# Performance work log

Hardware: AMD Instinct MI355X
Metric: run time of the kernel (lower is better)

## Reference

```python
import jax, jax.numpy as jnp
import numpy as np

D_MODEL = 512
NUM_HEADS = 8
NUM_REL_EMB = 1024


def _linear(x, w, b):
    # torch nn.Linear convention: w is [out, in]
    return x @ w.T + b


def setup_inputs() -> dict:
    key = jax.random.key(0)
    B, S, D = 1, 512, D_MODEL
    ks = jax.random.split(key, 14)
    scale = D ** -0.5
    def w(i):
        return jax.random.normal(ks[i], (D, D), jnp.float32) * scale
    def b(i):
        return jax.random.normal(ks[i], (D,), jnp.float32) * 0.01
    return {
        "hidden_states": jax.random.normal(ks[0], (B, S, D), jnp.float32),
        "emb_table": jax.random.normal(ks[1], (NUM_REL_EMB, D), jnp.float32) * 0.02,
        "wq": w(2), "bq": b(3),
        "wk": w(4), "bk": b(5),
        "wv": w(6), "bv": b(7),
        "wrk": w(8), "brk": b(9),
        "wrq": w(10), "brq": b(11),
        "wo": w(12), "bo": b(13),
    }


def reference(hidden_states, emb_table, wq, bq, wk, bk, wv, bv,
              wrk, brk, wrq, brq, wo, bo):
    B, S, D = hidden_states.shape
    H = NUM_HEADS
    hd = D // H
    NE = emb_table.shape[0]

    # relative positions j - i, shifted and clamped, then embedded: [S, S, D]
    rel_pos = jnp.arange(S)[None, :] - jnp.arange(S)[:, None]
    idx = jnp.clip(rel_pos + NE // 2, 0, NE - 1)
    rel_emb = emb_table[idx]  # [S, S, D] (identical across batch)

    q = _linear(hidden_states, wq, bq).reshape(B, S, H, hd).transpose(0, 2, 1, 3)  # [B,H,S,hd]
    k = _linear(hidden_states, wk, bk).reshape(B, S, H, hd).transpose(0, 2, 1, 3)
    v = _linear(hidden_states, wv, bv).reshape(B, S, H, hd).transpose(0, 2, 1, 3)

    rk = _linear(rel_emb, wrk, brk).reshape(S, S, H, hd)  # [i, j, H, hd]
    rq = _linear(rel_emb, wrq, brq).reshape(S, S, H, hd)

    # content-content + content-relative + relative-content scores: [B,H,S,S]
    scores = (
        jnp.einsum('bhid,bhjd->bhij', q, k)
        + jnp.einsum('bhid,ijhd->bhij', q, rk)
        + jnp.einsum('ijhd,bhjd->bhij', rq, k)
    )

    attn = jax.nn.softmax(scores / jnp.sqrt(jnp.asarray(hd, scores.dtype)), axis=-1)
    # dropout is identity (p=0.0 / eval mode)

    ctx = jnp.einsum('bhij,bhjd->bhid', attn, v)          # [B,H,S,hd]
    ctx = ctx.transpose(0, 2, 1, 3).reshape(B, S, D)       # merge heads
    out = _linear(ctx, wo, bo)
    return out, attn
```

## Files before the change

kernel.cpp:

```cpp
#include <hip/hip_runtime.h>
#include <stdint.h>


typedef __bf16 bf16_t;
typedef bf16_t bf16x8 __attribute__((ext_vector_type(8)));
typedef float f32x4 __attribute__((ext_vector_type(4)));

__device__ __forceinline__ uint16_t f2bf(float f) {
  union { float f; uint32_t i; } c; c.f = f;
  return (uint16_t)((c.i + 0x7fffu + ((c.i >> 16) & 1u)) >> 16);
}
__device__ __forceinline__ uint32_t pack2bf(float lo, float hi) {
  return (uint32_t)f2bf(lo) | ((uint32_t)f2bf(hi) << 16);
}
#define MFMA(a, b, c) __builtin_amdgcn_mfma_f32_16x16x32_bf16((a), (b), (c), 0, 0, 0)

#define LSTR 40
#define SSTR 72

__global__ __launch_bounds__(256) void gemm_bt_kernel(
    const void* __restrict__ A, int lda, int zsA, int aF32,
    const void* __restrict__ B, int ldb, int zsB, int bF32,
    const float* __restrict__ bias, int hasBias,
    float* __restrict__ C, int ldc, int zsC, int K)
{
  __shared__ __align__(16) uint16_t As[64 * LSTR];
  __shared__ __align__(16) uint16_t Bs[64 * LSTR];
  const int z = blockIdx.z;
  const int m0 = blockIdx.y * 64, n0 = blockIdx.x * 64;
  const int t = threadIdx.x, lane = t & 63, wave = t >> 6;
  const int wi = wave & 1, wj = wave >> 1;
  const int quad = lane >> 4, l15 = lane & 15;
  const int srow = t >> 2, scol = (t & 3) * 8;

  f32x4 acc[2][2] = {};
  for (int k0 = 0; k0 < K; k0 += 32) {
    uint4 ap, bp;
    if (aF32) {
      const float* Af = (const float*)A + (size_t)z * zsA + (size_t)(m0 + srow) * lda + (k0 + scol);
      float4 x0 = *(const float4*)(Af); float4 x1 = *(const float4*)(Af + 4);
      ap.x = pack2bf(x0.x, x0.y); ap.y = pack2bf(x0.z, x0.w);
      ap.z = pack2bf(x1.x, x1.y); ap.w = pack2bf(x1.z, x1.w);
    } else {
      ap = *(const uint4*)((const uint16_t*)A + (size_t)z * zsA + (size_t)(m0 + srow) * lda + (k0 + scol));
    }
    if (bF32) {
      const float* Bf = (const float*)B + (size_t)z * zsB + (size_t)(n0 + srow) * ldb + (k0 + scol);
      float4 x0 = *(const float4*)(Bf); float4 x1 = *(const float4*)(Bf + 4);
      bp.x = pack2bf(x0.x, x0.y); bp.y = pack2bf(x0.z, x0.w);
      bp.z = pack2bf(x1.x, x1.y); bp.w = pack2bf(x1.z, x1.w);
    } else {
      bp = *(const uint4*)((const uint16_t*)B + (size_t)z * zsB + (size_t)(n0 + srow) * ldb + (k0 + scol));
    }
    *(uint4*)(&As[srow * LSTR + scol]) = ap;
    *(uint4*)(&Bs[srow * LSTR + scol]) = bp;
    __syncthreads();
    bf16x8 af[2], bfr[2];
#pragma unroll
    for (int x = 0; x < 2; x++) {
      af[x]  = *(const bf16x8*)(&As[(wi * 32 + x * 16 + l15) * LSTR + quad * 8]);
      bfr[x] = *(const bf16x8*)(&Bs[(wj * 32 + x * 16 + l15) * LSTR + quad * 8]);
    }
#pragma unroll
    for (int x = 0; x < 2; x++)
#pragma unroll
      for (int y = 0; y < 2; y++)
        acc[x][y] = MFMA(af[x], bfr[y], acc[x][y]);
    __syncthreads();
  }
#pragma unroll
  for (int x = 0; x < 2; x++)
#pragma unroll
    for (int y = 0; y < 2; y++) {
      const int j = n0 + wj * 32 + y * 16 + l15;
      const float bval = hasBias ? bias[j] : 0.0f;
      const int ib = m0 + wi * 32 + x * 16 + quad * 4;
#pragma unroll
      for (int r = 0; r < 4; r++)
        C[(size_t)z * zsC + (size_t)(ib + r) * ldc + j] = acc[x][y][r] + bval;
    }
}

__global__ __launch_bounds__(256) void proj_kernel(
    const float* __restrict__ X, const float* __restrict__ emb,
    const float* __restrict__ wq, const float* __restrict__ bq,
    const float* __restrict__ wk, const float* __restrict__ bk,
    const float* __restrict__ wv, const float* __restrict__ bv,
    const float* __restrict__ wrk, const float* __restrict__ brk,
    const float* __restrict__ wrq, const float* __restrict__ brq,
    uint16_t* __restrict__ q, uint16_t* __restrict__ k, uint16_t* __restrict__ vT,
    uint16_t* __restrict__ rkE, uint16_t* __restrict__ rqE)
{
  int bid = blockIdx.x;
  const float *A, *B, *bias; uint16_t* C; int mode;
  if (bid < 64)       {            A = X;   B = wq;  bias = bq;  C = q;   mode = 2; }
  else if (bid < 128) { bid -= 64; A = X;   B = wk;  bias = bk;  C = k;   mode = 2; }
  else if (bid < 192) { bid -= 128; A = X;  B = wv;  bias = bv;  C = vT;  mode = 3; }
  else if (bid < 320) { bid -= 192; A = emb; B = wrk; bias = brk; C = rkE; mode = 1; }
  else                { bid -= 320; A = emb; B = wrq; bias = brq; C = rqE; mode = 1; }
  const int m0 = (bid >> 3) * 64, n0 = (bid & 7) * 64;

  __shared__ __align__(16) uint16_t As[64 * LSTR];
  __shared__ __align__(16) uint16_t Bs[64 * LSTR];
  const int t = threadIdx.x, lane = t & 63, wave = t >> 6;
  const int wi = wave & 1, wj = wave >> 1;
  const int quad = lane >> 4, l15 = lane & 15;
  const int srow = t >> 2, scol = (t & 3) * 8;

  f32x4 acc[2][2] = {};
  for (int k0 = 0; k0 < 512; k0 += 32) {
    const float* Af = A + (size_t)(m0 + srow) * 512 + (k0 + scol);
    const float* Bf = B + (size_t)(n0 + srow) * 512 + (k0 + scol);
    float4 a0 = *(const float4*)(Af), a1 = *(const float4*)(Af + 4);
    float4 b0 = *(const float4*)(Bf), b1 = *(const float4*)(Bf + 4);
    uint4 ap, bp;
    ap.x = pack2bf(a0.x, a0.y); ap.y = pack2bf(a0.z, a0.w);
    ap.z = pack2bf(a1.x, a1.y); ap.w = pack2bf(a1.z, a1.w);
    bp.x = pack2bf(b0.x, b0.y); bp.y = pack2bf(b0.z, b0.w);
    bp.z = pack2bf(b1.x, b1.y); bp.w = pack2bf(b1.z, b1.w);
    *(uint4*)(&As[srow * LSTR + scol]) = ap;
    *(uint4*)(&Bs[srow * LSTR + scol]) = bp;
    __syncthreads();
    bf16x8 af[2], bfr[2];
#pragma unroll
    for (int x = 0; x < 2; x++) {
      af[x]  = *(const bf16x8*)(&As[(wi * 32 + x * 16 + l15) * LSTR + quad * 8]);
      bfr[x] = *(const bf16x8*)(&Bs[(wj * 32 + x * 16 + l15) * LSTR + quad * 8]);
    }
#pragma unroll
    for (int x = 0; x < 2; x++)
#pragma unroll
      for (int y = 0; y < 2; y++)
        acc[x][y] = MFMA(af[x], bfr[y], acc[x][y]);
    __syncthreads();
  }
#pragma unroll
  for (int x = 0; x < 2; x++)
#pragma unroll
    for (int y = 0; y < 2; y++) {
      const int j = n0 + wj * 32 + y * 16 + l15;
      const float bval = bias[j];
      const int ib = m0 + wi * 32 + x * 16 + quad * 4;
#pragma unroll
      for (int r = 0; r < 4; r++) {
        const int i = ib + r;
        size_t off;
        if (mode == 1)      off = (size_t)i * 512 + j;
        else if (mode == 2) off = (size_t)(j >> 6) * 32768 + (size_t)i * 64 + (size_t)(j & 63);
        else                off = (size_t)(j >> 6) * 32768 + (size_t)(j & 63) * 512 + (size_t)i;
        C[off] = f2bf(acc[x][y][r] + bval);
      }
    }
}

__global__ __launch_bounds__(256) void scores_kernel(
    const uint16_t* __restrict__ q, const uint16_t* __restrict__ k,
    const uint16_t* __restrict__ rkE, const uint16_t* __restrict__ rqE,
    float* __restrict__ S)
{
  __shared__ __align__(16) char smem[67072];
  uint16_t* stg = (uint16_t*)smem;
  float* U2 = (float*)smem;
  float* U3 = U2 + 64 * 130;

  const int h = blockIdx.y;
  const int i0 = (blockIdx.x >> 3) * 64, j0 = (blockIdx.x & 7) * 64;
  const int ebase = j0 - i0 + 449;
  const int t = threadIdx.x, lane = t & 63, w = t >> 6;
  const int quad = lane >> 4, l15 = lane & 15;

  for (int idx = t; idx < 3072; idx += 256) {
    const int row = idx >> 3, c = (idx & 7) * 8;
    const uint16_t* src;
    if (row < 64)       src = q   + (size_t)h * 32768 + (size_t)(i0 + row) * 64 + c;
    else if (row < 128) src = k   + (size_t)h * 32768 + (size_t)(j0 + row - 64) * 64 + c;
    else if (row < 256) src = rqE + (size_t)(ebase + row - 128) * 512 + h * 64 + c;
    else                src = rkE + (size_t)(ebase + row - 256) * 512 + h * 64 + c;
    *(uint4*)(&stg[row * SSTR + c]) = *(const uint4*)src;
  }
  __syncthreads();

  f32x4 acc1[4] = {}, acc2[8] = {}, acc3[2][4] = {};
#pragma unroll
  for (int s = 0; s < 2; s++) {
    const int ko = s * 32 + quad * 8;
    bf16x8 aq = *(const bf16x8*)(&stg[(w * 16 + l15) * SSTR + ko]);
    bf16x8 bk[4], arq[2], brk[8];
#pragma unroll
    for (int tt = 0; tt < 4; tt++) bk[tt]  = *(const bf16x8*)(&stg[(64 + tt * 16 + l15) * SSTR + ko]);
#pragma unroll
    for (int x = 0; x < 2; x++)    arq[x]  = *(const bf16x8*)(&stg[(128 + w * 32 + x * 16 + l15) * SSTR + ko]);
#pragma unroll
    for (int tt = 0; tt < 8; tt++) brk[tt] = *(const bf16x8*)(&stg[(256 + tt * 16 + l15) * SSTR + ko]);
#pragma unroll
    for (int tt = 0; tt < 4; tt++) acc1[tt] = MFMA(aq, bk[tt], acc1[tt]);
#pragma unroll
    for (int tt = 0; tt < 8; tt++) acc2[tt] = MFMA(aq, brk[tt], acc2[tt]);
#pragma unroll
    for (int x = 0; x < 2; x++)
#pragma unroll
      for (int tt = 0; tt < 4; tt++) acc3[x][tt] = MFMA(arq[x], bk[tt], acc3[x][tt]);
  }
  __syncthreads();
#pragma unroll
  for (int tt = 0; tt < 8; tt++)
#pragma unroll
    for (int r = 0; r < 4; r++)
      U2[(w * 16 + quad * 4 + r) * 130 + tt * 16 + l15] = acc2[tt][r];
#pragma unroll
  for (int x = 0; x < 2; x++)
#pragma unroll
    for (int tt = 0; tt < 4; tt++)
#pragma unroll
      for (int r = 0; r < 4; r++)
        U3[(w * 32 + x * 16 + quad * 4 + r) * 66 + tt * 16 + l15] = acc3[x][tt][r];
  __syncthreads();
#pragma unroll
  for (int tt = 0; tt < 4; tt++)
#pragma unroll
    for (int r = 0; r < 4; r++) {
      const int ii = w * 16 + quad * 4 + r, jj = tt * 16 + l15;
      const int rb = jj - ii + 63;
      const float val = (acc1[tt][r] + U2[ii * 130 + rb] + U3[rb * 66 + jj]) * 0.125f;
      S[((size_t)h * 512 + i0 + ii) * 512 + j0 + jj] = val;
    }
}

__global__ __launch_bounds__(256) void softmax_kernel(
    const float* __restrict__ S, float* __restrict__ attn, uint16_t* __restrict__ attn_bf)
{
  const int t = threadIdx.x, lane = t & 63, w = t >> 6;
  const size_t row = (size_t)blockIdx.x * 4 + w;
  const float* Sr = S + row * 512 + lane * 8;
  float4 a = *(const float4*)Sr, b = *(const float4*)(Sr + 4);
  float v[8] = {a.x, a.y, a.z, a.w, b.x, b.y, b.z, b.w};
  float m = v[0];
#pragma unroll
  for (int i = 1; i < 8; i++) m = fmaxf(m, v[i]);
#pragma unroll
  for (int o = 32; o > 0; o >>= 1) m = fmaxf(m, __shfl_xor(m, o, 64));
  float p[8], sum = 0.f;
#pragma unroll
  for (int i = 0; i < 8; i++) { p[i] = __expf(v[i] - m); sum += p[i]; }
#pragma unroll
  for (int o = 32; o > 0; o >>= 1) sum += __shfl_xor(sum, o, 64);
  const float inv = 1.0f / sum;
#pragma unroll
  for (int i = 0; i < 8; i++) p[i] *= inv;
  float* Ar = attn + row * 512 + lane * 8;
  *(float4*)Ar       = make_float4(p[0], p[1], p[2], p[3]);
  *(float4*)(Ar + 4) = make_float4(p[4], p[5], p[6], p[7]);
  uint4 pk;
  pk.x = pack2bf(p[0], p[1]); pk.y = pack2bf(p[2], p[3]);
  pk.z = pack2bf(p[4], p[5]); pk.w = pack2bf(p[6], p[7]);
  *(uint4*)(attn_bf + row * 512 + lane * 8) = pk;
}

extern "C" void kernel_launch(void* const* d_in, const int* in_sizes, int n_in,
                              void* d_out, int out_size, void* d_ws, size_t ws_size,
                              hipStream_t stream) {
  const float* X   = (const float*)d_in[0];
  const float* emb = (const float*)d_in[1];
  const float* wq  = (const float*)d_in[2];
  const float* bq  = (const float*)d_in[3];
  const float* wk  = (const float*)d_in[4];
  const float* bk  = (const float*)d_in[5];
  const float* wv  = (const float*)d_in[6];
  const float* bv  = (const float*)d_in[7];
  const float* wrk = (const float*)d_in[8];
  const float* brk = (const float*)d_in[9];
  const float* wrq = (const float*)d_in[10];
  const float* brq = (const float*)d_in[11];
  const float* wo  = (const float*)d_in[12];
  const float* bo  = (const float*)d_in[13];

  uint16_t* q       = (uint16_t*)d_ws;
  uint16_t* k       = q   + 262144;
  uint16_t* vT      = k   + 262144;
  uint16_t* rkE     = vT  + 262144;
  uint16_t* rqE     = rkE + 524288;
  uint16_t* attn_bf = rqE + 524288;
  float*    S       = (float*)(attn_bf + 2097152);
  float*    ctx     = S + 2097152;

  float* outp = (float*)d_out;
  float* attn = (float*)d_out + 262144;

  const dim3 blk(256);
  proj_kernel<<<dim3(448), blk, 0, stream>>>(X, emb, wq, bq, wk, bk, wv, bv,
                                             wrk, brk, wrq, brq, q, k, vT, rkE, rqE);
  scores_kernel<<<dim3(64, 8), blk, 0, stream>>>(q, k, rkE, rqE, S);
  softmax_kernel<<<dim3(1024), blk, 0, stream>>>(S, attn, attn_bf);
  gemm_bt_kernel<<<dim3(1, 8, 8), blk, 0, stream>>>(attn_bf, 512, 262144, 0,
                                                    vT, 512, 32768, 0,
                                                    nullptr, 0, ctx, 512, 64, 512);
  gemm_bt_kernel<<<dim3(8, 8, 1), blk, 0, stream>>>(ctx, 512, 0, 1,
                                                    wo, 512, 0, 1,
                                                    bo, 1, outp, 512, 0, 512);
}
```

Measured before the change: 143.8 us.

## Fuse scores, softmax and attn·V into one attention kernel per row block

Replaces the separate scores, softmax and attn@V GEMM kernels with one kernel. Each block owns a 64-row strip of one head, loops over all key tiles keeping scores in registers, runs softmax in place, writes attn, and multiplies the probabilities by V into a bf16 context. This removes the fp32 score buffer round trip, the bf16 attn copy and two launches. The cost is that only 64 blocks of 256 threads run with very high register use (sc[8][4] f32x4), so occupancy and parallelism on a large GPU are low. The kernel also reads V directly from global memory inside the MFMA loop.

```diff
diff --git a/kernel.cpp b/kernel.cpp
--- a/kernel.cpp
+++ b/kernel.cpp
@@ -153,107 +153,156 @@
     }
 }
 
-__global__ __launch_bounds__(256) void scores_kernel(
+__global__ __launch_bounds__(256, 1) void attn_fused_kernel(
     const uint16_t* __restrict__ q, const uint16_t* __restrict__ k,
     const uint16_t* __restrict__ rkE, const uint16_t* __restrict__ rqE,
-    float* __restrict__ S)
+    const uint16_t* __restrict__ vT,
+    float* __restrict__ attn, uint16_t* __restrict__ ctx_bf)
 {
-  __shared__ __align__(16) char smem[67072];
-  uint16_t* stg = (uint16_t*)smem;
-  float* U2 = (float*)smem;
+  __shared__ __align__(16) char smem[85504];
+  uint16_t* qs  = (uint16_t*)smem;
+  uint16_t* stg = (uint16_t*)(smem + 9216);
+  float* U2 = (float*)(smem + 9216);
   float* U3 = U2 + 64 * 130;
-
-  const int h = blockIdx.y;
-  const int i0 = (blockIdx.x >> 3) * 64, j0 = (blockIdx.x & 7) * 64;
-  const int ebase = j0 - i0 + 449;
+  uint16_t* Pb = (uint16_t*)(smem + 76288);
+
+  const int h = blockIdx.y, i0 = blockIdx.x * 64;
   const int t = threadIdx.x, lane = t & 63, w = t >> 6;
   const int quad = lane >> 4, l15 = lane & 15;
 
-  for (int idx = t; idx < 3072; idx += 256) {
-    const int row = idx >> 3, c = (idx & 7) * 8;
-    const uint16_t* src;
-    if (row < 64)       src = q   + (size_t)h * 32768 + (size_t)(i0 + row) * 64 + c;
-    else if (row < 128) src = k   + (size_t)h * 32768 + (size_t)(j0 + row - 64) * 64 + c;
-    else if (row < 256) src = rqE + (size_t)(ebase + row - 128) * 512 + h * 64 + c;
-    else                src = rkE + (size_t)(ebase + row - 256) * 512 + h * 64 + c;
-    *(uint4*)(&stg[row * SSTR + c]) = *(const uint4*)src;
-  }
-  __syncthreads();
-
-  f32x4 acc1[4] = {}, acc2[8] = {}, acc3[2][4] = {};
-#pragma unroll
-  for (int s = 0; s < 2; s++) {
-    const int ko = s * 32 + quad * 8;
-    bf16x8 aq = *(const bf16x8*)(&stg[(w * 16 + l15) * SSTR + ko]);
-    bf16x8 bk[4], arq[2], brk[8];
-#pragma unroll
-    for (int tt = 0; tt < 4; tt++) bk[tt]  = *(const bf16x8*)(&stg[(64 + tt * 16 + l15) * SSTR + ko]);
-#pragma unroll
-    for (int x = 0; x < 2; x++)    arq[x]  = *(const bf16x8*)(&stg[(128 + w * 32 + x * 16 + l15) * SSTR + ko]);
-#pragma unroll
-    for (int tt = 0; tt < 8; tt++) brk[tt] = *(const bf16x8*)(&stg[(256 + tt * 16 + l15) * SSTR + ko]);
-#pragma unroll
-    for (int tt = 0; tt < 4; tt++) acc1[tt] = MFMA(aq, bk[tt], acc1[tt]);
-#pragma unroll
-    for (int tt = 0; tt < 8; tt++) acc2[tt] = MFMA(aq, brk[tt], acc2[tt]);
+#pragma unroll
+  for (int c = 0; c < 2; c++) {
+    const int idx = t + c * 256, row = idx >> 3, col = (idx & 7) * 8;
+    *(uint4*)(&qs[row * SSTR + col]) =
+        *(const uint4*)(q + (size_t)h * 32768 + (size_t)(i0 + row) * 64 + col);
+  }
+
+  f32x4 sc[8][4];
+#pragma unroll
+  for (int jt = 0; jt < 8; jt++) {
+    const int j0 = jt * 64;
+    const int ebase = j0 - i0 + 449;
+    __syncthreads();
+#pragma unroll
+    for (int c = 0; c < 10; c++) {
+      const int idx = t + c * 256, row = idx >> 3, col = (idx & 7) * 8;
+      const uint16_t* src;
+      if (row < 64)       src = k   + (size_t)h * 32768 + (size_t)(j0 + row) * 64 + col;
+      else if (row < 192) src = rqE + (size_t)min(ebase + row - 64, 1023) * 512 + h * 64 + col;
+      else                src = rkE + (size_t)min(ebase + row - 192, 1023) * 512 + h * 64 + col;
+      *(uint4*)(&stg[row * SSTR + col]) = *(const uint4*)src;
+    }
+    __syncthreads();
+
+    f32x4 acc1[4] = {}, acc2[8] = {}, acc3[2][4] = {};
+#pragma unroll
+    for (int s = 0; s < 2; s++) {
+      const int ko = s * 32 + quad * 8;
+      bf16x8 aq = *(const bf16x8*)(&qs[(w * 16 + l15) * SSTR + ko]);
+      bf16x8 bk[4], arq[2], brk[8];
+#pragma unroll
+      for (int tt = 0; tt < 4; tt++) bk[tt]  = *(const bf16x8*)(&stg[(tt * 16 + l15) * SSTR + ko]);
+#pragma unroll
+      for (int x = 0; x < 2; x++)    arq[x]  = *(const bf16x8*)(&stg[(64 + w * 32 + x * 16 + l15) * SSTR + ko]);
+#pragma unroll
+      for (int tt = 0; tt < 8; tt++) brk[tt] = *(const bf16x8*)(&stg[(192 + tt * 16 + l15) * SSTR + ko]);
+#pragma unroll
+      for (int tt = 0; tt < 4; tt++) acc1[tt] = MFMA(aq, bk[tt], acc1[tt]);
+#pragma unroll
+      for (int tt = 0; tt < 8; tt++) acc2[tt] = MFMA(aq, brk[tt], acc2[tt]);
+#pragma unroll
+      for (int x = 0; x < 2; x++)
+#pragma unroll
+        for (int tt = 0; tt < 4; tt++) acc3[x][tt] = MFMA(arq[x], bk[tt], acc3[x][tt]);
+    }
+    __syncthreads();
+#pragma unroll
+    for (int tt = 0; tt < 8; tt++)
+#pragma unroll
+      for (int r = 0; r < 4; r++)
+        U2[(w * 16 + quad * 4 + r) * 130 + tt * 16 + l15] = acc2[tt][r];
 #pragma unroll
     for (int x = 0; x < 2; x++)
 #pragma unroll
-      for (int tt = 0; tt < 4; tt++) acc3[x][tt] = MFMA(arq[x], bk[tt], acc3[x][tt]);
-  }
-  __syncthreads();
-#pragma unroll
-  for (int tt = 0; tt < 8; tt++)
+      for (int tt = 0; tt < 4; tt++)
+#pragma unroll
+        for (int r = 0; r < 4; r++)
+          U3[(w * 32 + x * 16 + quad * 4 + r) * 66 + tt * 16 + l15] = acc3[x][tt][r];
+    __syncthreads();
+#pragma unroll
+    for (int tt = 0; tt < 4; tt++)
+#pragma unroll
+      for (int r = 0; r < 4; r++) {
+        const int ii = w * 16 + quad * 4 + r, jj = tt * 16 + l15;
+        const int rb = jj - ii + 63;
+        sc[jt][tt][r] = (acc1[tt][r] + U2[ii * 130 + rb] + U3[rb * 66 + jj]) * 0.125f;
+      }
+  }
+
+#pragma unroll
+  for (int r = 0; r < 4; r++) {
+    float m = -1e30f;
+#pragma unroll
+    for (int jt = 0; jt < 8; jt++)
+#pragma unroll
+      for (int tt = 0; tt < 4; tt++) m = fmaxf(m, sc[jt][tt][r]);
+#pragma unroll
+    for (int o = 1; o < 16; o <<= 1) m = fmaxf(m, __shfl_xor(m, o, 64));
+    float sum = 0.f;
+#pragma unroll
+    for (int jt = 0; jt < 8; jt++)
+#pragma unroll
+      for (int tt = 0; tt < 4; tt++) {
+        const float p = __expf(sc[jt][tt][r] - m);
+        sc[jt][tt][r] = p; sum += p;
+      }
+#pragma unroll
+    for (int o = 1; o < 16; o <<= 1) sum += __shfl_xor(sum, o, 64);
+    const float inv = 1.0f / sum;
+#pragma unroll
+    for (int jt = 0; jt < 8; jt++)
+#pragma unroll
+      for (int tt = 0; tt < 4; tt++) sc[jt][tt][r] *= inv;
+  }
+
+#pragma unroll
+  for (int jt = 0; jt < 8; jt++)
+#pragma unroll
+    for (int tt = 0; tt < 4; tt++)
+#pragma unroll
+      for (int r = 0; r < 4; r++)
+        attn[((size_t)h * 512 + i0 + w * 16 + quad * 4 + r) * 512 + jt * 64 + tt * 16 + l15]
+            = sc[jt][tt][r];
+
+  f32x4 apv[4] = {};
+  uint16_t* Pw = Pb + w * 16 * SSTR;
+#pragma unroll
+  for (int jt = 0; jt < 8; jt++) {
+    __syncthreads();
+#pragma unroll
+    for (int tt = 0; tt < 4; tt++)
+#pragma unroll
+      for (int r = 0; r < 4; r++)
+        Pw[(quad * 4 + r) * SSTR + tt * 16 + l15] = f2bf(sc[jt][tt][r]);
+    __syncthreads();
+#pragma unroll
+    for (int s = 0; s < 2; s++) {
+      const int ko = s * 32 + quad * 8;
+      bf16x8 aP = *(const bf16x8*)(&Pw[l15 * SSTR + ko]);
+#pragma unroll
+      for (int tt = 0; tt < 4; tt++) {
+        bf16x8 bv = *(const bf16x8*)(vT + (size_t)h * 32768 + (size_t)(tt * 16 + l15) * 512
+                                     + jt * 64 + ko);
+        apv[tt] = MFMA(aP, bv, apv[tt]);
+      }
+    }
+  }
+#pragma unroll
+  for (int tt = 0; tt < 4; tt++)
 #pragma unroll
     for (int r = 0; r < 4; r++)
-      U2[(w * 16 + quad * 4 + r) * 130 + tt * 16 + l15] = acc2[tt][r];
-#pragma unroll
-  for (int x = 0; x < 2; x++)
-#pragma unroll
-    for (int tt = 0; tt < 4; tt++)
-#pragma unroll
-      for (int r = 0; r < 4; r++)
-        U3[(w * 32 + x * 16 + quad * 4 + r) * 66 + tt * 16 + l15] = acc3[x][tt][r];
-  __syncthreads();
-#pragma unroll
-  for (int tt = 0; tt < 4; tt++)
-#pragma unroll
-    for (int r = 0; r < 4; r++) {
-      const int ii = w * 16 + quad * 4 + r, jj = tt * 16 + l15;
-      const int rb = jj - ii + 63;
-      const float val = (acc1[tt][r] + U2[ii * 130 + rb] + U3[rb * 66 + jj]) * 0.125f;
-      S[((size_t)h * 512 + i0 + ii) * 512 + j0 + jj] = val;
-    }
-}
-
-__global__ __launch_bounds__(256) void softmax_kernel(
-    const float* __restrict__ S, float* __restrict__ attn, uint16_t* __restrict__ attn_bf)
-{
-  const int t = threadIdx.x, lane = t & 63, w = t >> 6;
-  const size_t row = (size_t)blockIdx.x * 4 + w;
-  const float* Sr = S + row * 512 + lane * 8;
-  float4 a = *(const float4*)Sr, b = *(const float4*)(Sr + 4);
-  float v[8] = {a.x, a.y, a.z, a.w, b.x, b.y, b.z, b.w};
-  float m = v[0];
-#pragma unroll
-  for (int i = 1; i < 8; i++) m = fmaxf(m, v[i]);
-#pragma unroll
-  for (int o = 32; o > 0; o >>= 1) m = fmaxf(m, __shfl_xor(m, o, 64));
-  float p[8], sum = 0.f;
-#pragma unroll
-  for (int i = 0; i < 8; i++) { p[i] = __expf(v[i] - m); sum += p[i]; }
-#pragma unroll
-  for (int o = 32; o > 0; o >>= 1) sum += __shfl_xor(sum, o, 64);
-  const float inv = 1.0f / sum;
-#pragma unroll
-  for (int i = 0; i < 8; i++) p[i] *= inv;
-  float* Ar = attn + row * 512 + lane * 8;
-  *(float4*)Ar       = make_float4(p[0], p[1], p[2], p[3]);
-  *(float4*)(Ar + 4) = make_float4(p[4], p[5], p[6], p[7]);
-  uint4 pk;
-  pk.x = pack2bf(p[0], p[1]); pk.y = pack2bf(p[2], p[3]);
-  pk.z = pack2bf(p[4], p[5]); pk.w = pack2bf(p[6], p[7]);
-  *(uint4*)(attn_bf + row * 512 + lane * 8) = pk;
+      ctx_bf[(size_t)(i0 + w * 16 + quad * 4 + r) * 512 + h * 64 + tt * 16 + l15]
+          = f2bf(apv[tt][r]);
 }
 
 extern "C" void kernel_launch(void* const* d_in, const int* in_sizes, int n_in,
@@ -274,14 +323,12 @@
   const float* wo  = (const float*)d_in[12];
   const float* bo  = (const float*)d_in[13];
 
-  uint16_t* q       = (uint16_t*)d_ws;
-  uint16_t* k       = q   + 262144;
-  uint16_t* vT      = k   + 262144;
-  uint16_t* rkE     = vT  + 262144;
-  uint16_t* rqE     = rkE + 524288;
-  uint16_t* attn_bf = rqE + 524288;
-  float*    S       = (float*)(attn_bf + 2097152);
-  float*    ctx     = S + 2097152;
+  uint16_t* q      = (uint16_t*)d_ws;
+  uint16_t* k      = q   + 262144;
+  uint16_t* vT     = k   + 262144;
+  uint16_t* rkE    = vT  + 262144;
+  uint16_t* rqE    = rkE + 524288;
+  uint16_t* ctx_bf = rqE + 524288;
 
   float* outp = (float*)d_out;
   float* attn = (float*)d_out + 262144;
@@ -289,12 +336,8 @@
   const dim3 blk(256);
   proj_kernel<<<dim3(448), blk, 0, stream>>>(X, emb, wq, bq, wk, bk, wv, bv,
                                              wrk, brk, wrq, brq, q, k, vT, rkE, rqE);
-  scores_kernel<<<dim3(64, 8), blk, 0, stream>>>(q, k, rkE, rqE, S);
-  softmax_kernel<<<dim3(1024), blk, 0, stream>>>(S, attn, attn_bf);
-  gemm_bt_kernel<<<dim3(1, 8, 8), blk, 0, stream>>>(attn_bf, 512, 262144, 0,
-                                                    vT, 512, 32768, 0,
-                                                    nullptr, 0, ctx, 512, 64, 512);
-  gemm_bt_kernel<<<dim3(8, 8, 1), blk, 0, stream>>>(ctx, 512, 0, 1,
+  attn_fused_kernel<<<dim3(8, 8), blk, 0, stream>>>(q, k, rkE, rqE, vT, attn, ctx_bf);
+  gemm_bt_kernel<<<dim3(8, 8, 1), blk, 0, stream>>>(ctx_bf, 512, 0, 0,
                                                     wo, 512, 0, 1,
                                                     bo, 1, outp, 512, 0, 512);
 }
```

Result: slower. 166.7 us (+15.9%).
